# Kernel tuning notes

Measured on AMD Instinct MI355X. Metric: run time of the kernel, lower is better.

The kernel has to match this reference:

```python
import jax, jax.numpy as jnp
import numpy as np

E, T, H, I, K = 16, 2048, 1024, 512, 2  # experts, tokens, hidden, intermediate, top_k


def setup_inputs() -> dict:
    key = jax.random.key(0)
    k1, k2, k3, k4, k5 = jax.random.split(key, 5)
    hidden_states = jax.random.normal(k1, (T, H), dtype=jnp.float32)
    topk_weights = jax.random.uniform(k2, (T, K), dtype=jnp.float32)
    topk_indices = jax.random.randint(k3, (T, K), 0, E, dtype=jnp.int32)
    # learned expert params, viewed per expert as in _view_experts_weight()
    gate_up_proj = jax.random.normal(k4, (E, H, 2 * I), dtype=jnp.float32) * 0.02
    down_proj = jax.random.normal(k5, (E, I, H), dtype=jnp.float32) * 0.02
    return {
        "hidden_states": hidden_states,
        "topk_weights": topk_weights,
        "topk_indices": topk_indices,
        "gate_up_proj": gate_up_proj,
        "down_proj": down_proj,
    }


def reference(hidden_states, topk_weights, topk_indices, gate_up_proj, down_proj):
    """MoE experts: per-expert gate_up GEMM -> silu-gate -> down GEMM,
    combined with top-k routing weights (index_add over tokens in the original).

    Equivalent dense formulation: combine[e, t] = sum_k topk_weights[t, k] * [topk_indices[t, k] == e];
    out = sum_e expert_e(hidden_states) * combine[e][:, None]. Tokens not routed to e get
    weight 0, matching the original gather/scatter-add exactly (including duplicate
    expert ids within a token, which accumulate).
    """
    num_experts = gate_up_proj.shape[0]
    one_hot = jax.nn.one_hot(topk_indices, num_experts, dtype=topk_weights.dtype)  # [T, K, E]
    combine = jnp.einsum("tk,tke->et", topk_weights, one_hot)  # [E, T]

    def body(acc, xs):
        w_gu, w_d, w = xs  # [H, 2I], [I, H], [T]
        gate_up = hidden_states @ w_gu  # [T, 2I]
        gate, up = jnp.split(gate_up, 2, axis=-1)
        expert_out = (jax.nn.silu(gate) * up) @ w_d  # [T, H]
        return acc + expert_out * w[:, None], None

    init = jnp.zeros_like(hidden_states)
    out, _ = jax.lax.scan(body, init, (gate_up_proj, down_proj, combine))
    return out.astype(hidden_states.dtype)
```

## Files before the change

### kernel.cpp

```cpp
#include <hip/hip_runtime.h>

#define E_ 16
#define T_ 2048
#define H_ 1024
#define I_ 512
#define NPAIR 4096
#define BM 128
#define MAXTILE 48

typedef __bf16 bf16x8 __attribute__((ext_vector_type(8)));
typedef float  f32x4  __attribute__((ext_vector_type(4)));

static __device__ __forceinline__ unsigned short f2bf(float f) {
    __bf16 h = (__bf16)f;
    return __builtin_bit_cast(unsigned short, h);
}

static __device__ __forceinline__ uint4 pack8(const float* v) {
    union { unsigned short us[8]; uint4 u; } r;
    #pragma unroll
    for (int i = 0; i < 8; ++i) r.us[i] = f2bf(v[i]);
    return r.u;
}

static __device__ __forceinline__ void gl_lds16(const void* g, void* l) {
    __builtin_amdgcn_global_load_lds(
        (const __attribute__((address_space(1))) unsigned int*)g,
        (__attribute__((address_space(3))) unsigned int*)l,
        16, 0, 0);
}

__global__ __launch_bounds__(256) void route_kernel(
    const float* __restrict__ tw, const int* __restrict__ ti,
    int* __restrict__ offs, int* __restrict__ tile_e, int* __restrict__ tile_r,
    int* __restrict__ pair_ts, float* __restrict__ pair_w)
{
    __shared__ unsigned short hist[256][E_];
    __shared__ int ebase[E_];
    const int tid = threadIdx.x;

    int e_loc[16];
    unsigned short h[E_];
    for (int e = 0; e < E_; ++e) h[e] = 0;
    for (int i = 0; i < 16; ++i) {
        int p = tid * 16 + i;
        int e = ti[p];
        e_loc[i] = e;
        h[e]++;
    }
    for (int e = 0; e < E_; ++e) hist[tid][e] = h[e];
    __syncthreads();

    if (tid < E_) {
        int e = tid, run = 0;
        for (int t = 0; t < 256; ++t) {
            unsigned short c = hist[t][e];
            hist[t][e] = (unsigned short)run;
            run += c;
        }
        ebase[e] = run;
    }
    __syncthreads();
    if (tid == 0) {
        int run = 0, nt = 0;
        for (int e = 0; e < E_; ++e) {
            int c = ebase[e];
            offs[e] = run; ebase[e] = run;
            for (int r = 0; r < c; r += BM) { tile_e[nt] = e; tile_r[nt] = r; ++nt; }
            run += c;
        }
        offs[E_] = run;
        for (; nt < MAXTILE; ++nt) tile_e[nt] = -1;
    }
    __syncthreads();

    int cur[E_];
    for (int e = 0; e < E_; ++e) cur[e] = ebase[e] + hist[tid][e];
    for (int i = 0; i < 16; ++i) {
        int p = tid * 16 + i;
        int e = e_loc[i];
        int pos = cur[e]++;
        pair_ts[pos] = p;
        pair_w[pos]  = tw[p];
    }
}

__global__ __launch_bounds__(256) void gather_kernel(
    const float* __restrict__ X, const int* __restrict__ pair_ts,
    unsigned short* __restrict__ Ag)
{
    const int q = blockIdx.x;
    const int t = pair_ts[q] >> 1;
    const int c = threadIdx.x * 4;
    const float4 x = *(const float4*)&X[(size_t)t * H_ + c];
    ushort4 b; b.x = f2bf(x.x); b.y = f2bf(x.y); b.z = f2bf(x.z); b.w = f2bf(x.w);
    *(ushort4*)&Ag[(size_t)q * H_ + c] = b;
}

#define MFMA_TILE(AS, BS)                                                              \
    _Pragma("unroll")                                                                  \
    for (int kkj = 0; kkj < 2; ++kkj) {                                                \
        const int j0 = kkj * 4;                                                        \
        bf16x8 af[4], bfr[2];                                                          \
        _Pragma("unroll")                                                              \
        for (int m = 0; m < 4; ++m)                                                    \
            af[m] = *(const bf16x8*)&AS[wm * 64 + m * 16 + lrow][((j0 + lk) ^ (lrow & 7)) * 8]; \
        _Pragma("unroll")                                                              \
        for (int n = 0; n < 2; ++n)                                                    \
            bfr[n] = *(const bf16x8*)&BS[wn * 32 + n * 16 + lrow][((j0 + lk) ^ (lrow & 7)) * 8]; \
        _Pragma("unroll")                                                              \
        for (int m = 0; m < 4; ++m)                                                    \
            _Pragma("unroll")                                                          \
            for (int n = 0; n < 2; ++n)                                                \
                acc[m][n] = __builtin_amdgcn_mfma_f32_16x16x32_bf16(af[m], bfr[n], acc[m][n], 0, 0, 0); \
    }

#define ISSUE_BV(BV, KB, BSTRIDE)                                                      \
    _Pragma("unroll")                                                                  \
    for (int i = 0; i < 16; ++i)                                                       \
        BV[i] = bsrc[(size_t)((KB) + w * 16 + i) * (BSTRIDE)];

#define ISSUE_A(BUF, KB)                                                               \
    _Pragma("unroll")                                                                  \
    for (int i = 0; i < 4; ++i) gl_lds16(asrc[i] + (KB), &BUF[w * 32 + i * 8][0]);

#define PACK_B(BS, BV)                                                                 \
    *(uint4*)&BS[bn][bg0] = pack8(&(BV)[0]);                                           \
    *(uint4*)&BS[bn][bg1] = pack8(&(BV)[8]);

#define K_PIPELINE(NT, BSTRIDE)                                                        \
    float bv0[16], bv1[16], bv2[16], bv3[16];                                          \
    ISSUE_BV(bv0, 0, BSTRIDE)                                                          \
    PACK_B(Bs[0], bv0)                                                                 \
    ISSUE_A(As[0], 0)                                                                  \
    __builtin_amdgcn_sched_barrier(0);                                                 \
    ISSUE_BV(bv1, 64, BSTRIDE)                                                         \
    ISSUE_A(As[1], 64)                                                                 \
    asm volatile("s_waitcnt vmcnt(20) lgkmcnt(0)" ::: "memory");                       \
    asm volatile("s_barrier" ::: "memory");                                            \
    _Pragma("unroll")                                                                  \
    for (int j = 0; j < (NT); ++j) {                                                   \
        if (j + 2 < (NT)) {                                                            \
            if (((j + 2) & 3) == 0) { ISSUE_BV(bv0, (j + 2) * 64, BSTRIDE) }           \
            if (((j + 2) & 3) == 1) { ISSUE_BV(bv1, (j + 2) * 64, BSTRIDE) }           \
            if (((j + 2) & 3) == 2) { ISSUE_BV(bv2, (j + 2) * 64, BSTRIDE) }           \
            if (((j + 2) & 3) == 3) { ISSUE_BV(bv3, (j + 2) * 64, BSTRIDE) }           \
            ISSUE_A(As[(j + 2) % 3], (j + 2) * 64)                                     \
        }                                                                              \
        if (j + 1 < (NT)) {                                                            \
            if (((j + 1) & 3) == 0) { PACK_B(Bs[(j + 1) & 1], bv0) }                   \
            if (((j + 1) & 3) == 1) { PACK_B(Bs[(j + 1) & 1], bv1) }                   \
            if (((j + 1) & 3) == 2) { PACK_B(Bs[(j + 1) & 1], bv2) }                   \
            if (((j + 1) & 3) == 3) { PACK_B(Bs[(j + 1) & 1], bv3) }                   \
        }                                                                              \
        __builtin_amdgcn_s_setprio(1);                                                 \
        MFMA_TILE(As[j % 3], Bs[j & 1])                                                \
        __builtin_amdgcn_s_setprio(0);                                                 \
        if (j + 2 < (NT)) {                                                            \
            asm volatile("s_waitcnt vmcnt(20) lgkmcnt(0)" ::: "memory");               \
            asm volatile("s_barrier" ::: "memory");                                    \
        } else if (j + 1 < (NT)) {                                                     \
            asm volatile("s_waitcnt vmcnt(0) lgkmcnt(0)" ::: "memory");                \
            asm volatile("s_barrier" ::: "memory");                                    \
        }                                                                              \
    }

__global__ __launch_bounds__(256, 2) void gemm1_kernel(
    const unsigned short* __restrict__ Ag, const float* __restrict__ W1,
    const int* __restrict__ offs, const int* __restrict__ tile_e,
    const int* __restrict__ tile_r, unsigned short* __restrict__ act)
{
    const int e = tile_e[blockIdx.y];
    if (e < 0) return;
    const int rbeg = offs[e], rend = offs[e + 1];
    const int ne   = rend - rbeg;
    const int row0 = tile_r[blockIdx.y];
    const int c0 = blockIdx.x * 32;

    __shared__ unsigned short As[3][128][64];
    __shared__ unsigned short Bs[2][64][64];

    const int tid  = threadIdx.x;
    const int lane = tid & 63;
    const int w    = tid >> 6;
    const int wm   = w >> 1, wn = w & 1;
    const int lrow = lane & 15;
    const int lk   = lane >> 4;

    const float* __restrict__ W1e = W1 + (size_t)e * (H_ * 2 * I_);

    const int r8 = lane >> 3, gr = lane & 7;
    const unsigned short* asrc[4];
    #pragma unroll
    for (int i = 0; i < 4; ++i) {
        int q = rbeg + row0 + w * 32 + i * 8 + r8;
        if (q > rend - 1) q = rend - 1;
        asrc[i] = Ag + (size_t)q * H_ + (gr ^ r8) * 8;
    }

    const int bn   = lane;
    const int bcol = ((bn >> 4) & 1) * I_ + c0 + (bn >> 5) * 16 + (bn & 15);
    const float* __restrict__ bsrc = W1e + bcol;
    const int bg0 = ((2 * w)     ^ (bn & 7)) * 8;
    const int bg1 = ((2 * w + 1) ^ (bn & 7)) * 8;

    f32x4 acc[4][2];
    #pragma unroll
    for (int m = 0; m < 4; ++m)
        #pragma unroll
        for (int n = 0; n < 2; ++n)
            acc[m][n] = f32x4{0.f, 0.f, 0.f, 0.f};

    K_PIPELINE(16, 2 * I_)

    for (int m = 0; m < 4; ++m) {
        #pragma unroll
        for (int reg = 0; reg < 4; ++reg) {
            int rloc = wm * 64 + m * 16 + lk * 4 + reg;
            if (row0 + rloc < ne) {
                int q = rbeg + row0 + rloc;
                float g = acc[m][0][reg], u = acc[m][1][reg];
                float a = g / (1.f + __expf(-g)) * u;
                act[(size_t)q * I_ + c0 + wn * 16 + lrow] = f2bf(a);
            }
        }
    }
}

__global__ __launch_bounds__(256, 2) void gemm2_kernel(
    const unsigned short* __restrict__ actg, const float* __restrict__ W2,
    const int* __restrict__ offs, const int* __restrict__ tile_e,
    const int* __restrict__ tile_r, const int* __restrict__ pair_ts,
    const float* __restrict__ pair_w, float* __restrict__ out)
{
    const int e = tile_e[blockIdx.y];
    if (e < 0) return;
    const int rbeg = offs[e], rend = offs[e + 1];
    const int ne   = rend - rbeg;
    const int row0 = tile_r[blockIdx.y];
    const int c0 = blockIdx.x * 64;

    __shared__ unsigned short As[3][128][64];
    __shared__ unsigned short Bs[2][64][64];

    const int tid  = threadIdx.x;
    const int lane = tid & 63;
    const int w    = tid >> 6;
    const int wm   = w >> 1, wn = w & 1;
    const int lrow = lane & 15;
    const int lk   = lane >> 4;

    const float* __restrict__ W2e = W2 + (size_t)e * (I_ * H_);

    const int r8 = lane >> 3, gr = lane & 7;
    const unsigned short* asrc[4];
    #pragma unroll
    for (int i = 0; i < 4; ++i) {
        int q = rbeg + row0 + w * 32 + i * 8 + r8;
        if (q > rend - 1) q = rend - 1;
        asrc[i] = actg + (size_t)q * I_ + (gr ^ r8) * 8;
    }

    const int bn = lane;
    const float* __restrict__ bsrc = W2e + c0 + bn;
    const int bg0 = ((2 * w)     ^ (bn & 7)) * 8;
    const int bg1 = ((2 * w + 1) ^ (bn & 7)) * 8;

    f32x4 acc[4][2];
    #pragma unroll
    for (int m = 0; m < 4; ++m)
        #pragma unroll
        for (int n = 0; n < 2; ++n)
            acc[m][n] = f32x4{0.f, 0.f, 0.f, 0.f};

    K_PIPELINE(8, H_)

    for (int m = 0; m < 4; ++m) {
        #pragma unroll
        for (int reg = 0; reg < 4; ++reg) {
            int rloc = wm * 64 + m * 16 + lk * 4 + reg;
            if (row0 + rloc < ne) {
                int q   = rbeg + row0 + rloc;
                int t   = pair_ts[q] >> 1;
                float wt = pair_w[q];
                #pragma unroll
                for (int n = 0; n < 2; ++n) {
                    int cg = c0 + wn * 32 + n * 16 + lrow;
                    atomicAdd(&out[(size_t)t * H_ + cg], wt * acc[m][n][reg]);
                }
            }
        }
    }
}

extern "C" void kernel_launch(void* const* d_in, const int* in_sizes, int n_in,
                              void* d_out, int out_size, void* d_ws, size_t ws_size,
                              hipStream_t stream)
{
    const float* X  = (const float*)d_in[0];
    const float* tw = (const float*)d_in[1];
    const int*   ti = (const int*)d_in[2];
    const float* W1 = (const float*)d_in[3];
    const float* W2 = (const float*)d_in[4];
    float* out = (float*)d_out;

    char* ws = (char*)d_ws;
    int*   offs    = (int*)(ws);
    int*   tile_e  = (int*)(ws + 128);
    int*   tile_r  = (int*)(ws + 128 + MAXTILE * 4);
    int*   pair_ts = (int*)(ws + 1024);
    float* pair_w  = (float*)(ws + 1024 + NPAIR * 4);
    unsigned short* Ag  = (unsigned short*)(ws + (1u << 16));
    unsigned short* act = (unsigned short*)(ws + (1u << 16) + (size_t)NPAIR * H_ * 2);

    hipMemsetAsync(d_out, 0, (size_t)out_size * sizeof(float), stream);

    route_kernel<<<1, 256, 0, stream>>>(tw, ti, offs, tile_e, tile_r, pair_ts, pair_w);

    gather_kernel<<<NPAIR, 256, 0, stream>>>(X, pair_ts, Ag);

    gemm1_kernel<<<dim3(I_ / 32, MAXTILE), 256, 0, stream>>>(Ag, W1, offs, tile_e, tile_r, act);

    gemm2_kernel<<<dim3(H_ / 64, MAXTILE), 256, 0, stream>>>(act, W2, offs, tile_e, tile_r, pair_ts, pair_w, out);
}
```

Baseline: 96.97 us.

## Stage fp32 weights into LDS via direct global-to-LDS loads, then transpose-pack

Weight tiles were previously loaded into registers with 16 strided scalar loads per thread and packed into bf16. They are now copied as fp32 straight into a new double-buffered LDS area using 16-byte global-to-LDS loads, and a separate pass reads them back from LDS and packs them into the bf16 B tile. The A staging drops from triple to double buffering and the wait/barrier schedule is rebuilt. This is meant to cut vector register pressure and use wide coalesced loads, at the cost of 32KB more LDS per block, which may lower occupancy, plus extra LDS traffic and barriers.

```diff
diff --git a/kernel.cpp b/kernel.cpp
--- a/kernel.cpp
+++ b/kernel.cpp
@@ -115,52 +115,53 @@
                 acc[m][n] = __builtin_amdgcn_mfma_f32_16x16x32_bf16(af[m], bfr[n], acc[m][n], 0, 0, 0); \
     }
 
-#define ISSUE_BV(BV, KB, BSTRIDE)                                                      \
+#define STAGE_A(BUF, KB)                                                               \
     _Pragma("unroll")                                                                  \
-    for (int i = 0; i < 16; ++i)                                                       \
-        BV[i] = bsrc[(size_t)((KB) + w * 16 + i) * (BSTRIDE)];
-
-#define ISSUE_A(BUF, KB)                                                               \
+    for (int i = 0; i < 4; ++i) gl_lds16(asrc[i] + (KB), &As[BUF][w * 32 + i * 8][0]);
+
+#define STAGE_W(BUF, KB, WSTRIDE)                                                      \
     _Pragma("unroll")                                                                  \
-    for (int i = 0; i < 4; ++i) gl_lds16(asrc[i] + (KB), &BUF[w * 32 + i * 8][0]);
-
-#define PACK_B(BS, BV)                                                                 \
-    *(uint4*)&BS[bn][bg0] = pack8(&(BV)[0]);                                           \
-    *(uint4*)&BS[bn][bg1] = pack8(&(BV)[8]);
-
-#define K_PIPELINE(NT, BSTRIDE)                                                        \
-    float bv0[16], bv1[16], bv2[16], bv3[16];                                          \
-    ISSUE_BV(bv0, 0, BSTRIDE)                                                          \
-    PACK_B(Bs[0], bv0)                                                                 \
-    ISSUE_A(As[0], 0)                                                                  \
-    __builtin_amdgcn_sched_barrier(0);                                                 \
-    ISSUE_BV(bv1, 64, BSTRIDE)                                                         \
-    ISSUE_A(As[1], 64)                                                                 \
-    asm volatile("s_waitcnt vmcnt(20) lgkmcnt(0)" ::: "memory");                       \
+    for (int i = 0; i < 4; ++i)                                                        \
+        gl_lds16(wsrc + (size_t)((KB) + w * 16 + i * 4 + kloc) * (WSTRIDE),            \
+                 &Wf[BUF][w * 16 + i * 4][0]);
+
+#define TRANSPOSE_W(CUR, NXT)                                                          \
+    {                                                                                  \
+        float tv[16];                                                                  \
+        _Pragma("unroll")                                                              \
+        for (int i = 0; i < 16; ++i) tv[i] = Wf[CUR][w * 16 + i][lane];                \
+        *(uint4*)&Bs[NXT][trow][tg0 * 8] = pack8(&tv[0]);                              \
+        *(uint4*)&Bs[NXT][trow][tg1 * 8] = pack8(&tv[8]);                              \
+    }
+
+#define K_PIPE(NT, WSTRIDE)                                                            \
+    STAGE_A(0, 0)                                                                      \
+    STAGE_W(1, 0, WSTRIDE)                                                             \
+    asm volatile("s_waitcnt vmcnt(0) lgkmcnt(0)" ::: "memory");                        \
+    asm volatile("s_barrier" ::: "memory");                                            \
+    TRANSPOSE_W(1, 0)                                                                  \
+    STAGE_W(0, 64, WSTRIDE)                                                            \
+    asm volatile("s_waitcnt lgkmcnt(0)" ::: "memory");                                 \
     asm volatile("s_barrier" ::: "memory");                                            \
     _Pragma("unroll")                                                                  \
     for (int j = 0; j < (NT); ++j) {                                                   \
+        const int cur = j & 1, nxt = cur ^ 1;                                          \
+        if (j + 1 < (NT)) STAGE_A(nxt, (j + 1) * 64)                                   \
+        if (j + 2 < (NT)) STAGE_W(nxt, (j + 2) * 64, WSTRIDE)                          \
         if (j + 2 < (NT)) {                                                            \
-            if (((j + 2) & 3) == 0) { ISSUE_BV(bv0, (j + 2) * 64, BSTRIDE) }           \
-            if (((j + 2) & 3) == 1) { ISSUE_BV(bv1, (j + 2) * 64, BSTRIDE) }           \
-            if (((j + 2) & 3) == 2) { ISSUE_BV(bv2, (j + 2) * 64, BSTRIDE) }           \
-            if (((j + 2) & 3) == 3) { ISSUE_BV(bv3, (j + 2) * 64, BSTRIDE) }           \
-            ISSUE_A(As[(j + 2) % 3], (j + 2) * 64)                                     \
+            asm volatile("s_waitcnt vmcnt(8)" ::: "memory");                           \
+        } else if (j + 1 < (NT)) {                                                     \
+            asm volatile("s_waitcnt vmcnt(4)" ::: "memory");                           \
+        } else {                                                                       \
+            asm volatile("s_waitcnt vmcnt(0)" ::: "memory");                           \
         }                                                                              \
+        asm volatile("s_barrier" ::: "memory");                                        \
+        if (j + 1 < (NT)) TRANSPOSE_W(cur, nxt)                                        \
+        __builtin_amdgcn_s_setprio(1);                                                 \
+        MFMA_TILE(As[cur], Bs[cur])                                                    \
+        __builtin_amdgcn_s_setprio(0);                                                 \
         if (j + 1 < (NT)) {                                                            \
-            if (((j + 1) & 3) == 0) { PACK_B(Bs[(j + 1) & 1], bv0) }                   \
-            if (((j + 1) & 3) == 1) { PACK_B(Bs[(j + 1) & 1], bv1) }                   \
-            if (((j + 1) & 3) == 2) { PACK_B(Bs[(j + 1) & 1], bv2) }                   \
-            if (((j + 1) & 3) == 3) { PACK_B(Bs[(j + 1) & 1], bv3) }                   \
-        }                                                                              \
-        __builtin_amdgcn_s_setprio(1);                                                 \
-        MFMA_TILE(As[j % 3], Bs[j & 1])                                                \
-        __builtin_amdgcn_s_setprio(0);                                                 \
-        if (j + 2 < (NT)) {                                                            \
-            asm volatile("s_waitcnt vmcnt(20) lgkmcnt(0)" ::: "memory");               \
-            asm volatile("s_barrier" ::: "memory");                                    \
-        } else if (j + 1 < (NT)) {                                                     \
-            asm volatile("s_waitcnt vmcnt(0) lgkmcnt(0)" ::: "memory");                \
+            asm volatile("s_waitcnt lgkmcnt(0)" ::: "memory");                         \
             asm volatile("s_barrier" ::: "memory");                                    \
         }                                                                              \
     }
@@ -177,7 +178,8 @@
     const int row0 = tile_r[blockIdx.y];
     const int c0 = blockIdx.x * 32;
 
-    __shared__ unsigned short As[3][128][64];
+    __shared__ unsigned short As[2][128][64];
+    __shared__ float          Wf[2][64][64];
     __shared__ unsigned short Bs[2][64][64];
 
     const int tid  = threadIdx.x;
@@ -198,11 +200,18 @@
         asrc[i] = Ag + (size_t)q * H_ + (gr ^ r8) * 8;
     }
 
-    const int bn   = lane;
-    const int bcol = ((bn >> 4) & 1) * I_ + c0 + (bn >> 5) * 16 + (bn & 15);
-    const float* __restrict__ bsrc = W1e + bcol;
-    const int bg0 = ((2 * w)     ^ (bn & 7)) * 8;
-    const int bg1 = ((2 * w + 1) ^ (bn & 7)) * 8;
+    const int nf   = (lane & 15) * 4;
+    const int kloc = lane >> 4;
+    const float* __restrict__ wsrc =
+        W1e + ((nf < 32) ? (c0 + nf) : (I_ + c0 + (nf - 32)));
+
+    {
+    }
+    const int tq   = lane >> 4;
+    const int tqr  = ((tq & 1) << 1) | (tq >> 1);
+    const int trow = tqr * 16 + (lane & 15);
+    const int tg0  = (2 * w)     ^ (trow & 7);
+    const int tg1  = (2 * w + 1) ^ (trow & 7);
 
     f32x4 acc[4][2];
     #pragma unroll
@@ -211,7 +220,7 @@
         for (int n = 0; n < 2; ++n)
             acc[m][n] = f32x4{0.f, 0.f, 0.f, 0.f};
 
-    K_PIPELINE(16, 2 * I_)
+    K_PIPE(16, 2 * I_)
 
     for (int m = 0; m < 4; ++m) {
         #pragma unroll
@@ -228,7 +237,7 @@
 }
 
 __global__ __launch_bounds__(256, 2) void gemm2_kernel(
-    const unsigned short* __restrict__ actg, const float* __restrict__ W2,
+    const unsigned short* __restrict__ Agact, const float* __restrict__ W2,
     const int* __restrict__ offs, const int* __restrict__ tile_e,
     const int* __restrict__ tile_r, const int* __restrict__ pair_ts,
     const float* __restrict__ pair_w, float* __restrict__ out)
@@ -240,7 +249,8 @@
     const int row0 = tile_r[blockIdx.y];
     const int c0 = blockIdx.x * 64;
 
-    __shared__ unsigned short As[3][128][64];
+    __shared__ unsigned short As[2][128][64];
+    __shared__ float          Wf[2][64][64];
     __shared__ unsigned short Bs[2][64][64];
 
     const int tid  = threadIdx.x;
@@ -258,13 +268,16 @@
     for (int i = 0; i < 4; ++i) {
         int q = rbeg + row0 + w * 32 + i * 8 + r8;
         if (q > rend - 1) q = rend - 1;
-        asrc[i] = actg + (size_t)q * I_ + (gr ^ r8) * 8;
-    }
-
-    const int bn = lane;
-    const float* __restrict__ bsrc = W2e + c0 + bn;
-    const int bg0 = ((2 * w)     ^ (bn & 7)) * 8;
-    const int bg1 = ((2 * w + 1) ^ (bn & 7)) * 8;
+        asrc[i] = Agact + (size_t)q * I_ + (gr ^ r8) * 8;
+    }
+
+    const int nf   = (lane & 15) * 4;
+    const int kloc = lane >> 4;
+    const float* __restrict__ wsrc = W2e + c0 + nf;
+
+    const int trow = lane;
+    const int tg0  = (2 * w)     ^ (trow & 7);
+    const int tg1  = (2 * w + 1) ^ (trow & 7);
 
     f32x4 acc[4][2];
     #pragma unroll
@@ -273,7 +286,7 @@
         for (int n = 0; n < 2; ++n)
             acc[m][n] = f32x4{0.f, 0.f, 0.f, 0.f};
 
-    K_PIPELINE(8, H_)
+    K_PIPE(8, H_)
 
     for (int m = 0; m < 4; ++m) {
         #pragma unroll
```

Measured after the change: 99.68 us. +2.8%, slower.
